# Kernel optimization log

Hardware: AMD Instinct MI355X
Metric: run time of the kernel (lower is better)

The kernel has to match this reference:

```python
import jax, jax.numpy as jnp
import numpy as np

D_EEG = 256; D_QUERY = 256; D_MODEL = 256; NUM_HEADS = 8
D_HEAD = D_MODEL // NUM_HEADS; PROJ_DIM = 40
B = 32; N = 4096


def _rope(x):
    # x: (B, S, H, D) -- rotate along sequence dim with interleaved-pair convention
    S, D = x.shape[1], x.shape[-1]
    inv = 1.0 / (10000.0 ** (jnp.arange(0, D, 2, dtype=jnp.float32) / D))
    f = jnp.arange(S, dtype=jnp.float32)[:, None] * inv[None, :]        # (S, D/2)
    cos = jnp.repeat(jnp.cos(f), 2, axis=-1)[None, :, None, :]
    sin = jnp.repeat(jnp.sin(f), 2, axis=-1)[None, :, None, :]
    xp = x.reshape(x.shape[:-1] + (D // 2, 2))
    rot = jnp.stack([-xp[..., 1], xp[..., 0]], axis=-1).reshape(x.shape)
    return x * cos + rot * sin


def _ln(x, g, b):
    m = x.mean(-1, keepdims=True)
    v = x.var(-1, keepdims=True)
    return (x - m) / jnp.sqrt(v + 1e-5) * g + b


def _l2norm(x):
    return x / jnp.maximum(jnp.linalg.norm(x, axis=-1, keepdims=True), 1e-12)


def setup_inputs():
    key = jax.random.key(0)
    ks = jax.random.split(key, 16)

    def lin(k, din, dout):
        s = 1.0 / np.sqrt(din)
        w = jax.random.uniform(k, (din, dout), minval=-s, maxval=s, dtype=jnp.float32)
        b = jax.random.uniform(jax.random.fold_in(k, 1), (dout,), minval=-s, maxval=s, dtype=jnp.float32)
        return w, b

    eeg_w, eeg_b = lin(ks[0], D_EEG, D_MODEL)
    stim_w, stim_b = lin(ks[1], D_QUERY, D_MODEL)
    temp_w, temp_b = lin(ks[2], D_QUERY, D_MODEL)
    q_w, q_b = lin(ks[3], D_MODEL, D_MODEL)
    k_w, k_b = lin(ks[4], D_MODEL, D_MODEL)
    v_w, v_b = lin(ks[5], D_MODEL, D_MODEL)
    fc_w, fc_b = lin(ks[6], D_MODEL, PROJ_DIM)

    return {
        "eeg_feat": jax.random.normal(ks[7], (B, N, D_EEG), dtype=jnp.float32),
        "stim_feat": jax.random.normal(ks[8], (B, D_QUERY), dtype=jnp.float32),
        "temp_feat": jax.random.normal(ks[9], (B, D_QUERY), dtype=jnp.float32),
        "eeg_w": eeg_w, "eeg_b": eeg_b,
        "stim_w": stim_w, "stim_b": stim_b,
        "temp_w": temp_w, "temp_b": temp_b,
        "q_w": q_w, "q_b": q_b,
        "k_w": k_w, "k_b": k_b,
        "v_w": v_w, "v_b": v_b,
        "fc_w": fc_w, "fc_b": fc_b,
        "lnq_g": jnp.ones((D_MODEL,), jnp.float32), "lnq_b": jnp.zeros((D_MODEL,), jnp.float32),
        "lnk_g": jnp.ones((D_MODEL,), jnp.float32), "lnk_b": jnp.zeros((D_MODEL,), jnp.float32),
    }


def reference(eeg_feat, stim_feat, temp_feat, eeg_w, eeg_b, stim_w, stim_b,
              temp_w, temp_b, q_w, q_b, k_w, k_b, v_w, v_b, fc_w, fc_b,
              lnq_g, lnq_b, lnk_g, lnk_b):
    Bq = eeg_feat.shape[0]
    eeg = eeg_feat @ eeg_w + eeg_b                      # (B, N, D)
    stim = (stim_feat @ stim_w + stim_b)[:, None, :]
    temp = (temp_feat @ temp_w + temp_b)[:, None, :]
    query = jnp.concatenate([stim, temp], axis=1)        # (B, 2, D)

    query = _ln(query, lnq_g, lnq_b)
    kv = _ln(eeg, lnk_g, lnk_b)

    Q = (query @ q_w + q_b).reshape(Bq, 2, NUM_HEADS, D_HEAD)
    K = (kv @ k_w + k_b).reshape(Bq, -1, NUM_HEADS, D_HEAD)
    V = (kv @ v_w + v_b).reshape(Bq, -1, NUM_HEADS, D_HEAD)

    Q = _l2norm(_rope(Q))
    K = _l2norm(_rope(K))

    scores = jnp.einsum('bqhd,bkhd->bhqk', Q, K) / np.sqrt(D_HEAD)
    scale = jax.lax.stop_gradient(
        jnp.maximum(jnp.std(scores, axis=-1, ddof=1, keepdims=True), 1e-3))
    scores = jnp.tanh(scores / (2.0 * scale)) * (5.0 * scale)

    w = jax.nn.softmax(scores, axis=-1)
    w = (w + 1e-4) / (w.sum(-1, keepdims=True) + 1e-8)

    attn_out = jnp.einsum('bhqk,bkhd->bqhd', w, V).reshape(Bq, 2, D_MODEL)
    pooled = attn_out.mean(axis=1)
    logits = pooled @ fc_w + fc_b
    return logits, pooled, attn_out, query
```

## Files before the change

kernel.cpp:

```cpp
#include <hip/hip_runtime.h>
#include <hip/hip_bf16.h>
#include <math.h>

#define TID ((int)threadIdx.x)

typedef float f32x4 __attribute__((ext_vector_type(4)));
typedef short s16x8 __attribute__((ext_vector_type(8)));

__device__ __forceinline__ unsigned short f2bf(float f) {
  union { float f; unsigned u; } v; v.f = f;
  unsigned r = v.u + 0x7FFFu + ((v.u >> 16) & 1u);
  return (unsigned short)(r >> 16);
}
__device__ __forceinline__ float bf2f(unsigned short h) {
  union { unsigned u; float f; } v; v.u = ((unsigned)h) << 16;
  return v.f;
}

__global__ __launch_bounds__(256) void prep1_kernel(
    const float* __restrict__ We, const float* __restrict__ Wk,
    const float* __restrict__ g, const float* __restrict__ be,
    const float* __restrict__ bln, const float* __restrict__ kb,
    unsigned short* __restrict__ wf, float2* __restrict__ trig,
    float* __restrict__ ckv, float* __restrict__ gkv, float* __restrict__ bkv) {
  int blk = blockIdx.x;
  if (blk < 32) {
    int fi = blk * 256 + TID;
    int l = fi & 63, ks = (fi >> 6) & 7, cbG = fi >> 9;
    int col = cbG * 16 + (l & 15);
    int kbase = ks * 32 + ((l >> 4) & 3) * 8;
    s16x8 pk;
#pragma unroll
    for (int e = 0; e < 8; ++e) pk[e] = (short)f2bf(We[(size_t)(kbase + e) * 256 + col]);
    *(s16x8*)&wf[(size_t)fi * 8] = pk;
  } else if (blk < 288) {
    int e = (blk - 32) * 256 + TID;
    int n = e >> 4, p = e & 15;
    float inv = exp2f(-(float)p * 0.8304820237218406f);
    float a = (float)n * inv;
    trig[e] = make_float2(cosf(a), sinf(a));
  } else {
    int j = TID;
    float a1 = 0.f, a2 = 0.f, a3 = 0.f;
    for (int k = 0; k < 256; ++k) {
      float wkj = Wk[k * 256 + j];
      float gk = g[k];
      a1 = fmaf(be[k] * gk, wkj, a1);
      a2 = fmaf(gk, wkj, a2);
      a3 = fmaf(bln[k], wkj, a3);
    }
    ckv[j] = a1; gkv[j] = a2; bkv[j] = a3 + kb[j];
  }
}

__global__ __launch_bounds__(256) void prep2_kernel(
    const float* __restrict__ We, const float* __restrict__ Wk,
    const float* __restrict__ g, unsigned short* __restrict__ wf) {
  int j = blockIdx.x;
  __shared__ float a[256];
  __shared__ float WeC[256 * 33];
  a[TID] = g[TID] * Wk[TID * 256 + j];
  float acc = 0.f;
  for (int k0 = 0; k0 < 256; k0 += 32) {
    __syncthreads();
    const float4* src = (const float4*)&We[TID * 256 + k0];
#pragma unroll
    for (int q4 = 0; q4 < 8; ++q4) {
      float4 v = src[q4];
      WeC[TID * 33 + q4 * 4 + 0] = v.x;
      WeC[TID * 33 + q4 * 4 + 1] = v.y;
      WeC[TID * 33 + q4 * 4 + 2] = v.z;
      WeC[TID * 33 + q4 * 4 + 3] = v.w;
    }
    __syncthreads();
#pragma unroll
    for (int kk = 0; kk < 32; ++kk)
      acc = fmaf(WeC[TID * 33 + kk], a[k0 + kk], acc);
  }
  int cbG = 16 + (j >> 4), c = j & 15;
  int ks = TID >> 5, g3 = (TID >> 3) & 3, e = TID & 7;
  size_t pos = (((size_t)(cbG * 8 + ks) * 64) + g3 * 16 + c) * 8 + e;
  wf[pos] = f2bf(acc);
}

__global__ __launch_bounds__(256) void q_kernel(
    const float* __restrict__ stim_feat, const float* __restrict__ temp_feat,
    const float* __restrict__ stim_w, const float* __restrict__ stim_b,
    const float* __restrict__ temp_w, const float* __restrict__ temp_b,
    const float* __restrict__ q_w, const float* __restrict__ q_b,
    const float* __restrict__ lnq_g, const float* __restrict__ lnq_b,
    float* __restrict__ out_query, float* __restrict__ qhat) {
  int b = blockIdx.x >> 1, q = blockIdx.x & 1;
  __shared__ float f[256];
  __shared__ float red[8];
  const float* feat = (q ? temp_feat : stim_feat) + b * 256;
  const float* W = q ? temp_w : stim_w;
  const float* bias = q ? temp_b : stim_b;
  f[TID] = feat[TID];
  __syncthreads();
  float acc = bias[TID];
#pragma unroll 8
  for (int i = 0; i < 256; ++i) acc = fmaf(f[i], W[i * 256 + TID], acc);
  float s1 = acc, s2 = acc * acc;
#pragma unroll
  for (int m = 1; m < 64; m <<= 1) { s1 += __shfl_xor(s1, m, 64); s2 += __shfl_xor(s2, m, 64); }
  if ((TID & 63) == 0) { red[TID >> 6] = s1; red[4 + (TID >> 6)] = s2; }
  __syncthreads();
  s1 = red[0] + red[1] + red[2] + red[3];
  s2 = red[4] + red[5] + red[6] + red[7];
  float mean = s1 * (1.f / 256.f);
  float var = s2 * (1.f / 256.f) - mean * mean;
  float rstd = rsqrtf(var + 1e-5f);
  float qln = (acc - mean) * rstd * lnq_g[TID] + lnq_b[TID];
  out_query[(b * 2 + q) * 256 + TID] = qln;
  __syncthreads();
  f[TID] = qln;
  __syncthreads();
  float a2 = q_b[TID];
#pragma unroll 8
  for (int i = 0; i < 256; ++i) a2 = fmaf(f[i], q_w[i * 256 + TID], a2);
  __syncthreads();
  f[TID] = a2;
  __syncthreads();
  float partner = f[TID ^ 1];
  int p = (TID >> 1) & 15;
  float inv = exp2f(-(float)p * 0.8304820237218406f);
  float ang = (float)q * inv;
  float cc_ = cosf(ang), ss_ = sinf(ang);
  float r = (TID & 1) ? fmaf(a2, cc_, partner * ss_) : fmaf(a2, cc_, -partner * ss_);
  float sq = r * r;
#pragma unroll
  for (int m = 1; m < 32; m <<= 1) sq += __shfl_xor(sq, m, 32);
  float rs = 1.f / fmaxf(sqrtf(sq), 1e-12f);
  qhat[(b * 2 + q) * 256 + TID] = r * rs;
}

__global__ __launch_bounds__(256) void main2_kernel(
    const float* __restrict__ x,
    const float* __restrict__ eeg_b,
    const unsigned short* __restrict__ wf,
    const float2* __restrict__ trig,
    const float* __restrict__ qhat,
    const float* __restrict__ ckv,
    const float* __restrict__ gkv,
    const float* __restrict__ bkv,
    float2* __restrict__ stats,
    float* __restrict__ scores) {

  __shared__ __align__(16) unsigned short A[32 * 256];
  __shared__ float CV0[256];
  __shared__ float CV1[256];
  __shared__ float CV2[256];
  __shared__ float QH[512];
  __shared__ float PS[32 * 9];
  __shared__ float2 ST[32];
  __shared__ float COS[32][17];
  __shared__ float SIN[32][17];

  const int tid = TID;
  const int w = tid >> 6, l = tid & 63, g = l >> 4, c = l & 15;
  const int r0 = blockIdx.x * 32;
  const int b = r0 >> 12;
  const int n0 = r0 & 4095;

#pragma unroll
  for (int i = 0; i < 4; ++i) {
    int ch = i * 256 + tid;
    int row = ch >> 5, cc = ch & 31;
    const float4* gp = (const float4*)(x + (size_t)(r0 + row) * 256 + cc * 8);
    float4 u0 = gp[0], u1 = gp[1];
    s16x8 pk;
    pk[0] = (short)f2bf(u0.x); pk[1] = (short)f2bf(u0.y);
    pk[2] = (short)f2bf(u0.z); pk[3] = (short)f2bf(u0.w);
    pk[4] = (short)f2bf(u1.x); pk[5] = (short)f2bf(u1.y);
    pk[6] = (short)f2bf(u1.z); pk[7] = (short)f2bf(u1.w);
    *(s16x8*)&A[row * 256 + ((cc ^ (row & 7)) * 8)] = pk;
  }
  {
    int trow = tid >> 4, p = tid & 15;
    float2 t0 = trig[(size_t)(n0 + trow) * 16 + p];
    float2 t1 = trig[(size_t)(n0 + 16 + trow) * 16 + p];
    COS[trow][p] = t0.x; SIN[trow][p] = t0.y;
    COS[16 + trow][p] = t1.x; SIN[16 + trow][p] = t1.y;
  }
  CV0[tid] = ckv[tid]; CV1[tid] = gkv[tid]; CV2[tid] = bkv[tid];
  QH[tid] = qhat[(size_t)b * 512 + tid];
  QH[256 + tid] = qhat[(size_t)b * 512 + 256 + tid];
  __syncthreads();

  f32x4 acc[2][8];
#pragma unroll
  for (int rb = 0; rb < 2; ++rb)
#pragma unroll
    for (int cb = 0; cb < 8; ++cb) acc[rb][cb] = (f32x4){0.f, 0.f, 0.f, 0.f};
#pragma unroll
  for (int ks = 0; ks < 8; ++ks) {
    s16x8 af[2];
#pragma unroll
    for (int rb = 0; rb < 2; ++rb) {
      int row = rb * 16 + c; int kc = ks * 4 + g;
      af[rb] = *(const s16x8*)&A[row * 256 + ((kc ^ (row & 7)) * 8)];
    }
#pragma unroll
    for (int hb = 0; hb < 2; ++hb) {
      s16x8 bf4[4];
#pragma unroll
      for (int q4 = 0; q4 < 4; ++q4) {
        int cbG = w * 8 + hb * 4 + q4;
        bf4[q4] = *(const s16x8*)&wf[(size_t)((cbG * 8 + ks) * 64 + l) * 8];
      }
#pragma unroll
      for (int rb = 0; rb < 2; ++rb)
#pragma unroll
        for (int q4 = 0; q4 < 4; ++q4)
          acc[rb][hb * 4 + q4] = __builtin_amdgcn_mfma_f32_16x16x32_bf16(
              af[rb], bf4[q4], acc[rb][hb * 4 + q4], 0, 0, 0);
    }
  }

  if (w < 2) {
    float ebias[8];
#pragma unroll
    for (int cb = 0; cb < 8; ++cb) ebias[cb] = eeg_b[w * 128 + cb * 16 + c];
    float ps[2][4], pq[2][4];
#pragma unroll
    for (int rb = 0; rb < 2; ++rb)
#pragma unroll
      for (int r = 0; r < 4; ++r) {
        float s = 0.f, q2 = 0.f;
#pragma unroll
        for (int cb = 0; cb < 8; ++cb) {
          float v = acc[rb][cb][r] + ebias[cb];
          s += v; q2 += v * v;
        }
        ps[rb][r] = s; pq[rb][r] = q2;
      }
#pragma unroll
    for (int m = 1; m < 16; m <<= 1)
#pragma unroll
      for (int rb = 0; rb < 2; ++rb)
#pragma unroll
        for (int r = 0; r < 4; ++r) {
          ps[rb][r] += __shfl_xor(ps[rb][r], m, 64);
          pq[rb][r] += __shfl_xor(pq[rb][r], m, 64);
        }
    float outS = 0.f, outQ = 0.f;
#pragma unroll
    for (int rb = 0; rb < 2; ++rb)
#pragma unroll
      for (int r = 0; r < 4; ++r)
        if (c == rb * 4 + r) { outS = ps[rb][r]; outQ = pq[rb][r]; }
    if (c < 8) {
      int row = (c >> 2) * 16 + g * 4 + (c & 3);
      PS[row * 9 + w * 2 + 0] = outS;
      PS[row * 9 + w * 2 + 1] = outQ;
    }
  }
  __syncthreads();

  if (tid < 32) {
    float s = PS[tid * 9 + 0] + PS[tid * 9 + 2];
    float q2 = PS[tid * 9 + 1] + PS[tid * 9 + 3];
    float mean = s * (1.f / 256.f);
    float var = q2 * (1.f / 256.f) - mean * mean;
    float rstd = rsqrtf(var + 1e-5f);
    ST[tid] = make_float2(mean, rstd);
    stats[(size_t)r0 + tid] = make_float2(mean, rstd);
  }
  if (w >= 2) {
#pragma unroll
    for (int rb = 0; rb < 2; ++rb)
#pragma unroll
      for (int r = 0; r < 4; ++r) {
        int row = rb * 16 + g * 4 + r;
#pragma unroll
        for (int cb = 0; cb < 8; ++cb) {
          int kcol = (w - 2) * 128 + cb * 16 + c;
          A[row * 256 + (kcol ^ ((row & 7) * 8))] = f2bf(acc[rb][cb][r]);
        }
      }
  }
  __syncthreads();

  {
    int h = tid >> 5, row = tid & 31;
    float2 st = ST[row];
    float is = st.y, mis = st.x * st.y;
    float ssq = 0.f, d0 = 0.f, d1 = 0.f;
#pragma unroll
    for (int j = 0; j < 4; ++j) {
      int u = h * 4 + j;
      s16x8 kvv = *(const s16x8*)&A[row * 256 + ((u ^ (row & 7)) * 8)];
#pragma unroll
      for (int t = 0; t < 4; ++t) {
        int col = h * 32 + j * 8 + 2 * t;
        int pp = j * 4 + t;
        float base0 = fmaf(CV0[col], is, fmaf(-mis, CV1[col], CV2[col]));
        float base1 = fmaf(CV0[col + 1], is, fmaf(-mis, CV1[col + 1], CV2[col + 1]));
        float k0 = fmaf(bf2f((unsigned short)kvv[2 * t]), is, base0);
        float k1 = fmaf(bf2f((unsigned short)kvv[2 * t + 1]), is, base1);
        float cx = COS[row][pp], sx = SIN[row][pp];
        float rv0 = k0 * cx - k1 * sx;
        float rv1 = fmaf(k1, cx, k0 * sx);
        ssq = fmaf(rv0, rv0, fmaf(rv1, rv1, ssq));
        d0 = fmaf(rv0, QH[col], fmaf(rv1, QH[col + 1], d0));
        d1 = fmaf(rv0, QH[256 + col], fmaf(rv1, QH[256 + col + 1], d1));
      }
    }
    float isv = 0.17677669529663687f / fmaxf(sqrtf(ssq), 1e-12f);
    scores[(size_t)((b * 8 + h) * 2 + 0) * 4096 + n0 + row] = d0 * isv;
    scores[(size_t)((b * 8 + h) * 2 + 1) * 4096 + n0 + row] = d1 * isv;
  }
}

__global__ __launch_bounds__(256) void wgt_kernel(
    const float* __restrict__ scores, const float2* __restrict__ stats,
    float* __restrict__ wbuf, float2* __restrict__ sbuf) {
  int b = blockIdx.x >> 3, h = blockIdx.x & 7;
  const float* s0p = scores + (size_t)((b * 8 + h) * 2 + 0) * 4096;
  const float* s1p = scores + (size_t)((b * 8 + h) * 2 + 1) * 4096;
  float sa[16], sb[16];
  float a1 = 0.f, a2 = 0.f, b1 = 0.f, b2 = 0.f;
#pragma unroll
  for (int i = 0; i < 16; ++i) {
    int k = i * 256 + TID;
    sa[i] = s0p[k]; sb[i] = s1p[k];
    a1 += sa[i]; a2 += sa[i] * sa[i];
    b1 += sb[i]; b2 += sb[i] * sb[i];
  }
  __shared__ float red[16];
  int w = TID >> 6;
#pragma unroll
  for (int m = 1; m < 64; m <<= 1) {
    a1 += __shfl_xor(a1, m, 64); a2 += __shfl_xor(a2, m, 64);
    b1 += __shfl_xor(b1, m, 64); b2 += __shfl_xor(b2, m, 64);
  }
  if ((TID & 63) == 0) { red[w * 4] = a1; red[w * 4 + 1] = a2; red[w * 4 + 2] = b1; red[w * 4 + 3] = b2; }
  __syncthreads();
  a1 = red[0] + red[4] + red[8] + red[12];
  a2 = red[1] + red[5] + red[9] + red[13];
  b1 = red[2] + red[6] + red[10] + red[14];
  b2 = red[3] + red[7] + red[11] + red[15];
  float va = (a2 - a1 * a1 * (1.f / 4096.f)) * (1.f / 4095.f);
  float vb = (b2 - b1 * b1 * (1.f / 4096.f)) * (1.f / 4095.f);
  float sga = fmaxf(sqrtf(fmaxf(va, 0.f)), 1e-3f);
  float sgb = fmaxf(sqrtf(fmaxf(vb, 0.f)), 1e-3f);
  float ia = 0.5f / sga, ib = 0.5f / sgb;
  float fa = 5.f * sga, fb = 5.f * sgb;
  float ea = 0.f, eb = 0.f;
#pragma unroll
  for (int i = 0; i < 16; ++i) {
    sa[i] = __expf(tanhf(sa[i] * ia) * fa);
    sb[i] = __expf(tanhf(sb[i] * ib) * fb);
    ea += sa[i]; eb += sb[i];
  }
#pragma unroll
  for (int m = 1; m < 64; m <<= 1) { ea += __shfl_xor(ea, m, 64); eb += __shfl_xor(eb, m, 64); }
  __syncthreads();
  if ((TID & 63) == 0) { red[w * 2] = ea; red[w * 2 + 1] = eb; }
  __syncthreads();
  ea = red[0] + red[2] + red[4] + red[6];
  eb = red[1] + red[3] + red[5] + red[7];
  float iea = 1.f / ea, ieb = 1.f / eb;
  float* w0 = wbuf + ((size_t)(b * 16) + h * 2 + 0) * 4096;
  float* w1 = w0 + 4096;
  float s1a = 0.f, s2a = 0.f, s1b = 0.f, s2b = 0.f;
#pragma unroll
  for (int i = 0; i < 16; ++i) {
    int k = i * 256 + TID;
    float2 st = stats[(size_t)b * 4096 + k];
    float wa = fmaf(sa[i], iea, 1e-4f);
    float wb = fmaf(sb[i], ieb, 1e-4f);
    float wta = wa * st.y, wtb = wb * st.y;
    w0[k] = wta; w1[k] = wtb;
    s1a += wta; s2a = fmaf(wta, st.x, s2a);
    s1b += wtb; s2b = fmaf(wtb, st.x, s2b);
  }
#pragma unroll
  for (int m = 1; m < 64; m <<= 1) {
    s1a += __shfl_xor(s1a, m, 64); s2a += __shfl_xor(s2a, m, 64);
    s1b += __shfl_xor(s1b, m, 64); s2b += __shfl_xor(s2b, m, 64);
  }
  __syncthreads();
  if ((TID & 63) == 0) { red[w * 4] = s1a; red[w * 4 + 1] = s2a; red[w * 4 + 2] = s1b; red[w * 4 + 3] = s2b; }
  __syncthreads();
  if (TID == 0) {
    sbuf[((size_t)(b * 8 + h)) * 2 + 0] =
        make_float2(red[0] + red[4] + red[8] + red[12], red[1] + red[5] + red[9] + red[13]);
    sbuf[((size_t)(b * 8 + h)) * 2 + 1] =
        make_float2(red[2] + red[6] + red[10] + red[14], red[3] + red[7] + red[11] + red[15]);
  }
}

__global__ __launch_bounds__(256) void ysum_kernel(
    const float* __restrict__ x, const float* __restrict__ wbuf,
    float* __restrict__ ypart) {
  int b = blockIdx.x >> 5, slab = blockIdx.x & 31;
  int h = TID >> 5, cg = TID & 31;
  const float* xb = x + ((size_t)(b * 4096 + slab * 128)) * 256 + cg * 8;
  const float* w0 = wbuf + ((size_t)(b * 16) + h * 2 + 0) * 4096 + slab * 128;
  const float* w1 = w0 + 4096;
  float y0[8], y1[8];
#pragma unroll
  for (int t = 0; t < 8; ++t) { y0[t] = 0.f; y1[t] = 0.f; }
#pragma unroll 4
  for (int r = 0; r < 128; ++r) {
    const float4* fp = (const float4*)(xb + (size_t)r * 256);
    float4 va = fp[0], vb4 = fp[1];
    float wa = w0[r], wc = w1[r];
    y0[0] = fmaf(wa, va.x, y0[0]);  y1[0] = fmaf(wc, va.x, y1[0]);
    y0[1] = fmaf(wa, va.y, y0[1]);  y1[1] = fmaf(wc, va.y, y1[1]);
    y0[2] = fmaf(wa, va.z, y0[2]);  y1[2] = fmaf(wc, va.z, y1[2]);
    y0[3] = fmaf(wa, va.w, y0[3]);  y1[3] = fmaf(wc, va.w, y1[3]);
    y0[4] = fmaf(wa, vb4.x, y0[4]); y1[4] = fmaf(wc, vb4.x, y1[4]);
    y0[5] = fmaf(wa, vb4.y, y0[5]); y1[5] = fmaf(wc, vb4.y, y1[5]);
    y0[6] = fmaf(wa, vb4.z, y0[6]); y1[6] = fmaf(wc, vb4.z, y1[6]);
    y0[7] = fmaf(wa, vb4.w, y0[7]); y1[7] = fmaf(wc, vb4.w, y1[7]);
  }
  float* yp = ypart + (((size_t)(b * 32 + slab) * 16) + h * 2) * 256 + cg * 8;
  *(float4*)&yp[0] = (float4){y0[0], y0[1], y0[2], y0[3]};
  *(float4*)&yp[4] = (float4){y0[4], y0[5], y0[6], y0[7]};
  *(float4*)&yp[256] = (float4){y1[0], y1[1], y1[2], y1[3]};
  *(float4*)&yp[260] = (float4){y1[4], y1[5], y1[6], y1[7]};
}

__global__ __launch_bounds__(256) void yz_kernel(
    const float* __restrict__ ypart, const float2* __restrict__ sbuf,
    const float* __restrict__ We, const float* __restrict__ be,
    const float* __restrict__ g, const float* __restrict__ bln,
    float* __restrict__ zbuf) {
  int b = blockIdx.x >> 4, hq = blockIdx.x & 15;
  __shared__ float Y[256];
  float s = 0.f;
#pragma unroll 8
  for (int sl = 0; sl < 32; ++sl)
    s += ypart[(((size_t)(b * 32 + sl) * 16) + hq) * 256 + TID];
  Y[TID] = s;
  __syncthreads();
  float2 s12 = sbuf[(size_t)b * 16 + hq];
  int k = TID;
  float t = s12.x * be[k];
#pragma unroll 8
  for (int cc = 0; cc < 256; ++cc)
    t = fmaf(Y[cc], We[cc * 256 + k], t);
  zbuf[((size_t)(b * 16) + hq) * 256 + k] = (t - s12.y) * g[k] + 1.4096f * bln[k];
}

__global__ __launch_bounds__(256) void att_kernel(
    const float* __restrict__ zbuf, const float* __restrict__ v_w,
    const float* __restrict__ v_b, float* __restrict__ out_attn,
    float* __restrict__ out_pooled) {
  int b = blockIdx.x >> 3, h = blockIdx.x & 7;
  __shared__ float ZA[2][256];
  __shared__ float ATTs[2][32];
  {
    int q = TID >> 7, cc = TID & 127;
    const float* zp = zbuf + ((size_t)(b * 16) + h * 2 + q) * 256;
    ZA[q][cc] = zp[cc];
    ZA[q][128 + cc] = zp[128 + cc];
  }
  __syncthreads();
  int q = TID >> 7, dl = (TID >> 2) & 31, quarter = TID & 3;
  int dout = h * 32 + dl;
  float ps = 0.f;
#pragma unroll 8
  for (int i = 0; i < 64; ++i) {
    int cc = quarter * 64 + i;
    ps = fmaf(ZA[q][cc], v_w[cc * 256 + dout], ps);
  }
  ps += __shfl_xor(ps, 1, 64);
  ps += __shfl_xor(ps, 2, 64);
  if (quarter == 0) {
    float val = ps + 1.4096f * v_b[dout];
    out_attn[(b * 2 + q) * 256 + dout] = val;
    ATTs[q][dl] = val;
  }
  __syncthreads();
  if (TID < 32) {
    out_pooled[b * 256 + h * 32 + TID] = 0.5f * (ATTs[0][TID] + ATTs[1][TID]);
  }
}

__global__ __launch_bounds__(256) void logit_kernel(
    const float* __restrict__ out_pooled, const float* __restrict__ fc_w,
    const float* __restrict__ fc_b, float* __restrict__ out_logits) {
  int b = blockIdx.x;
  __shared__ float P[256];
  P[TID] = out_pooled[b * 256 + TID];
  __syncthreads();
  if (TID < 40) {
    float acc = fc_b[TID];
#pragma unroll 8
    for (int i = 0; i < 256; ++i) acc = fmaf(P[i], fc_w[i * 40 + TID], acc);
    out_logits[b * 40 + TID] = acc;
  }
}

extern "C" void kernel_launch(void* const* d_in, const int* in_sizes, int n_in,
                              void* d_out, int out_size, void* d_ws, size_t ws_size,
                              hipStream_t stream) {
  (void)in_sizes; (void)n_in; (void)out_size; (void)ws_size;
  const float* eeg_feat  = (const float*)d_in[0];
  const float* stim_feat = (const float*)d_in[1];
  const float* temp_feat = (const float*)d_in[2];
  const float* eeg_w = (const float*)d_in[3];
  const float* eeg_b = (const float*)d_in[4];
  const float* stim_w = (const float*)d_in[5];
  const float* stim_b = (const float*)d_in[6];
  const float* temp_w = (const float*)d_in[7];
  const float* temp_b = (const float*)d_in[8];
  const float* q_w = (const float*)d_in[9];
  const float* q_b = (const float*)d_in[10];
  const float* k_w = (const float*)d_in[11];
  const float* k_b = (const float*)d_in[12];
  const float* v_w = (const float*)d_in[13];
  const float* v_b = (const float*)d_in[14];
  const float* fc_w = (const float*)d_in[15];
  const float* fc_b = (const float*)d_in[16];
  const float* lnq_g = (const float*)d_in[17];
  const float* lnq_b = (const float*)d_in[18];
  const float* lnk_g = (const float*)d_in[19];
  const float* lnk_b = (const float*)d_in[20];

  char* ws = (char*)d_ws;
  unsigned short* wfr = (unsigned short*)(ws + 0);
  float2* trig        = (float2*)(ws + 262144);
  float* qhat         = (float*)(ws + 786432);
  float* ckv          = (float*)(ws + 851968);
  float* gkv          = (float*)(ws + 852992);
  float* bkv          = (float*)(ws + 854016);
  float2* sbuf        = (float2*)(ws + 855040);
  float2* stats       = (float2*)(ws + 1048576);
  float* scores       = (float*)(ws + 2097152);
  float* wbuf         = (float*)(ws + 10485760);
  float* ypart        = (float*)(ws + 18874368);
  float* zbuf         = (float*)(ws + 35651584);

  float* out = (float*)d_out;
  float* out_logits = out;
  float* out_pooled = out + 1280;
  float* out_attn   = out + 9472;
  float* out_query  = out + 25856;

  prep1_kernel<<<289, 256, 0, stream>>>(eeg_w, k_w, lnk_g, eeg_b, lnk_b, k_b,
                                        wfr, trig, ckv, gkv, bkv);
  prep2_kernel<<<256, 256, 0, stream>>>(eeg_w, k_w, lnk_g, wfr);
  q_kernel<<<64, 256, 0, stream>>>(stim_feat, temp_feat, stim_w, stim_b,
                                   temp_w, temp_b, q_w, q_b, lnq_g, lnq_b,
                                   out_query, qhat);
  main2_kernel<<<4096, 256, 0, stream>>>(eeg_feat, eeg_b, wfr, trig, qhat,
                                         ckv, gkv, bkv, stats, scores);
  wgt_kernel<<<256, 256, 0, stream>>>(scores, stats, wbuf, sbuf);
  ysum_kernel<<<1024, 256, 0, stream>>>(eeg_feat, wbuf, ypart);
  yz_kernel<<<512, 256, 0, stream>>>(ypart, sbuf, eeg_w, eeg_b, lnk_g, lnk_b, zbuf);
  att_kernel<<<256, 256, 0, stream>>>(zbuf, v_w, v_b, out_attn, out_pooled);
  logit_kernel<<<32, 256, 0, stream>>>(out_pooled, fc_w, fc_b, out_logits);
}
```

Measured before the change: 217.1 us.

## Shrink main2 tile to 16 rows with 128-thread blocks, two waves over full width

Reworks the main fused GEMM+LN kernel so each block handles 16 rows with 128 threads instead of 32 rows with 256 threads. Each wave now computes all 256 columns of its half, wave 0 handling the eeg projection and LN stats and wave 1 the k projection, which removes the cross-wave partial-sum buffer and one reduction step. The grid doubles to 8192 blocks, giving more, smaller blocks for occupancy. In exchange, weight fragments are reloaded twice as often per row and each thread holds more accumulators, so register pressure rises.

```diff
diff --git a/kernel.cpp b/kernel.cpp
--- a/kernel.cpp
+++ b/kernel.cpp
@@ -135,7 +135,7 @@
   qhat[(b * 2 + q) * 256 + TID] = r * rs;
 }
 
-__global__ __launch_bounds__(256) void main2_kernel(
+__global__ __launch_bounds__(128) void main2_kernel(
     const float* __restrict__ x,
     const float* __restrict__ eeg_b,
     const unsigned short* __restrict__ wf,
@@ -147,25 +147,24 @@
     float2* __restrict__ stats,
     float* __restrict__ scores) {
 
-  __shared__ __align__(16) unsigned short A[32 * 256];
+  __shared__ __align__(16) unsigned short A[16 * 256];
   __shared__ float CV0[256];
   __shared__ float CV1[256];
   __shared__ float CV2[256];
   __shared__ float QH[512];
-  __shared__ float PS[32 * 9];
-  __shared__ float2 ST[32];
-  __shared__ float COS[32][17];
-  __shared__ float SIN[32][17];
+  __shared__ float2 ST[16];
+  __shared__ float COS[16][17];
+  __shared__ float SIN[16][17];
 
   const int tid = TID;
   const int w = tid >> 6, l = tid & 63, g = l >> 4, c = l & 15;
-  const int r0 = blockIdx.x * 32;
+  const int r0 = blockIdx.x * 16;
   const int b = r0 >> 12;
   const int n0 = r0 & 4095;
 
 #pragma unroll
   for (int i = 0; i < 4; ++i) {
-    int ch = i * 256 + tid;
+    int ch = i * 128 + tid;
     int row = ch >> 5, cc = ch & 31;
     const float4* gp = (const float4*)(x + (size_t)(r0 + row) * 256 + cc * 8);
     float4 u0 = gp[0], u1 = gp[1];
@@ -177,113 +176,90 @@
     *(s16x8*)&A[row * 256 + ((cc ^ (row & 7)) * 8)] = pk;
   }
   {
-    int trow = tid >> 4, p = tid & 15;
-    float2 t0 = trig[(size_t)(n0 + trow) * 16 + p];
-    float2 t1 = trig[(size_t)(n0 + 16 + trow) * 16 + p];
-    COS[trow][p] = t0.x; SIN[trow][p] = t0.y;
-    COS[16 + trow][p] = t1.x; SIN[16 + trow][p] = t1.y;
-  }
-  CV0[tid] = ckv[tid]; CV1[tid] = gkv[tid]; CV2[tid] = bkv[tid];
-  QH[tid] = qhat[(size_t)b * 512 + tid];
-  QH[256 + tid] = qhat[(size_t)b * 512 + 256 + tid];
-  __syncthreads();
-
-  f32x4 acc[2][8];
-#pragma unroll
-  for (int rb = 0; rb < 2; ++rb)
-#pragma unroll
-    for (int cb = 0; cb < 8; ++cb) acc[rb][cb] = (f32x4){0.f, 0.f, 0.f, 0.f};
+    int trow = tid >> 4, tp = tid & 15;
+    float2 t0 = trig[(size_t)(n0 + trow) * 16 + tp];
+    float2 t1 = trig[(size_t)(n0 + 8 + trow) * 16 + tp];
+    COS[trow][tp] = t0.x; SIN[trow][tp] = t0.y;
+    COS[8 + trow][tp] = t1.x; SIN[8 + trow][tp] = t1.y;
+  }
+  CV0[tid] = ckv[tid]; CV0[128 + tid] = ckv[128 + tid];
+  CV1[tid] = gkv[tid]; CV1[128 + tid] = gkv[128 + tid];
+  CV2[tid] = bkv[tid]; CV2[128 + tid] = bkv[128 + tid];
+#pragma unroll
+  for (int i = 0; i < 4; ++i) QH[i * 128 + tid] = qhat[(size_t)b * 512 + i * 128 + tid];
+  __syncthreads();
+
+  f32x4 acc[16];
+#pragma unroll
+  for (int cb = 0; cb < 16; ++cb) acc[cb] = (f32x4){0.f, 0.f, 0.f, 0.f};
 #pragma unroll
   for (int ks = 0; ks < 8; ++ks) {
-    s16x8 af[2];
-#pragma unroll
-    for (int rb = 0; rb < 2; ++rb) {
-      int row = rb * 16 + c; int kc = ks * 4 + g;
-      af[rb] = *(const s16x8*)&A[row * 256 + ((kc ^ (row & 7)) * 8)];
-    }
-#pragma unroll
-    for (int hb = 0; hb < 2; ++hb) {
+    int kc = ks * 4 + g;
+    s16x8 af = *(const s16x8*)&A[c * 256 + ((kc ^ (c & 7)) * 8)];
+#pragma unroll
+    for (int hb = 0; hb < 4; ++hb) {
       s16x8 bf4[4];
 #pragma unroll
       for (int q4 = 0; q4 < 4; ++q4) {
-        int cbG = w * 8 + hb * 4 + q4;
+        int cbG = w * 16 + hb * 4 + q4;
         bf4[q4] = *(const s16x8*)&wf[(size_t)((cbG * 8 + ks) * 64 + l) * 8];
       }
 #pragma unroll
-      for (int rb = 0; rb < 2; ++rb)
-#pragma unroll
-        for (int q4 = 0; q4 < 4; ++q4)
-          acc[rb][hb * 4 + q4] = __builtin_amdgcn_mfma_f32_16x16x32_bf16(
-              af[rb], bf4[q4], acc[rb][hb * 4 + q4], 0, 0, 0);
-    }
-  }
-
-  if (w < 2) {
-    float ebias[8];
-#pragma unroll
-    for (int cb = 0; cb < 8; ++cb) ebias[cb] = eeg_b[w * 128 + cb * 16 + c];
-    float ps[2][4], pq[2][4];
-#pragma unroll
-    for (int rb = 0; rb < 2; ++rb)
+      for (int q4 = 0; q4 < 4; ++q4)
+        acc[hb * 4 + q4] = __builtin_amdgcn_mfma_f32_16x16x32_bf16(af, bf4[q4], acc[hb * 4 + q4], 0, 0, 0);
+    }
+  }
+  __syncthreads();
+
+  if (w == 0) {
+    float ebias[16];
+#pragma unroll
+    for (int cb = 0; cb < 16; ++cb) ebias[cb] = eeg_b[cb * 16 + c];
+    float ps[4], pq[4];
+#pragma unroll
+    for (int r = 0; r < 4; ++r) {
+      float s = 0.f, q2 = 0.f;
+#pragma unroll
+      for (int cb = 0; cb < 16; ++cb) {
+        float v = acc[cb][r] + ebias[cb];
+        s += v; q2 += v * v;
+      }
+      ps[r] = s; pq[r] = q2;
+    }
+#pragma unroll
+    for (int m = 1; m < 16; m <<= 1)
 #pragma unroll
       for (int r = 0; r < 4; ++r) {
-        float s = 0.f, q2 = 0.f;
-#pragma unroll
-        for (int cb = 0; cb < 8; ++cb) {
-          float v = acc[rb][cb][r] + ebias[cb];
-          s += v; q2 += v * v;
-        }
-        ps[rb][r] = s; pq[rb][r] = q2;
+        ps[r] += __shfl_xor(ps[r], m, 64);
+        pq[r] += __shfl_xor(pq[r], m, 64);
       }
-#pragma unroll
-    for (int m = 1; m < 16; m <<= 1)
-#pragma unroll
-      for (int rb = 0; rb < 2; ++rb)
-#pragma unroll
-        for (int r = 0; r < 4; ++r) {
-          ps[rb][r] += __shfl_xor(ps[rb][r], m, 64);
-          pq[rb][r] += __shfl_xor(pq[rb][r], m, 64);
-        }
     float outS = 0.f, outQ = 0.f;
 #pragma unroll
-    for (int rb = 0; rb < 2; ++rb)
-#pragma unroll
-      for (int r = 0; r < 4; ++r)
-        if (c == rb * 4 + r) { outS = ps[rb][r]; outQ = pq[rb][r]; }
-    if (c < 8) {
-      int row = (c >> 2) * 16 + g * 4 + (c & 3);
-      PS[row * 9 + w * 2 + 0] = outS;
-      PS[row * 9 + w * 2 + 1] = outQ;
-    }
-  }
-  __syncthreads();
-
-  if (tid < 32) {
-    float s = PS[tid * 9 + 0] + PS[tid * 9 + 2];
-    float q2 = PS[tid * 9 + 1] + PS[tid * 9 + 3];
-    float mean = s * (1.f / 256.f);
-    float var = q2 * (1.f / 256.f) - mean * mean;
-    float rstd = rsqrtf(var + 1e-5f);
-    ST[tid] = make_float2(mean, rstd);
-    stats[(size_t)r0 + tid] = make_float2(mean, rstd);
-  }
-  if (w >= 2) {
-#pragma unroll
-    for (int rb = 0; rb < 2; ++rb)
-#pragma unroll
-      for (int r = 0; r < 4; ++r) {
-        int row = rb * 16 + g * 4 + r;
-#pragma unroll
-        for (int cb = 0; cb < 8; ++cb) {
-          int kcol = (w - 2) * 128 + cb * 16 + c;
-          A[row * 256 + (kcol ^ ((row & 7) * 8))] = f2bf(acc[rb][cb][r]);
-        }
+    for (int r = 0; r < 4; ++r)
+      if (c == r) { outS = ps[r]; outQ = pq[r]; }
+    if (c < 4) {
+      int row = g * 4 + c;
+      float mean = outS * (1.f / 256.f);
+      float var = outQ * (1.f / 256.f) - mean * mean;
+      float rstd = rsqrtf(var + 1e-5f);
+      ST[row] = make_float2(mean, rstd);
+      stats[(size_t)r0 + row] = make_float2(mean, rstd);
+    }
+  } else {
+#pragma unroll
+    for (int r = 0; r < 4; ++r) {
+      int row = g * 4 + r;
+#pragma unroll
+      for (int cb = 0; cb < 16; ++cb) {
+        int kcol = cb * 16 + c;
+        A[row * 256 + (kcol ^ ((row & 7) * 8))] = f2bf(acc[cb][r]);
       }
+    }
   }
   __syncthreads();
 
   {
-    int h = tid >> 5, row = tid & 31;
+    int h = tid >> 4, row = tid & 15;
     float2 st = ST[row];
     float is = st.y, mis = st.x * st.y;
     float ssq = 0.f, d0 = 0.f, d1 = 0.f;
@@ -548,7 +524,7 @@
   q_kernel<<<64, 256, 0, stream>>>(stim_feat, temp_feat, stim_w, stim_b,
                                    temp_w, temp_b, q_w, q_b, lnq_g, lnq_b,
                                    out_query, qhat);
-  main2_kernel<<<4096, 256, 0, stream>>>(eeg_feat, eeg_b, wfr, trig, qhat,
+  main2_kernel<<<8192, 128, 0, stream>>>(eeg_feat, eeg_b, wfr, trig, qhat,
                                          ckv, gkv, bkv, stats, scores);
   wgt_kernel<<<256, 256, 0, stream>>>(scores, stats, wbuf, sbuf);
   ysum_kernel<<<1024, 256, 0, stream>>>(eeg_feat, wbuf, ypart);
```

Measured after the change: 229.6 us. 1.06x slower.
